# Optimization experiments

Hardware: AMD Instinct MI355X
Metric: run time of the kernel (lower is better)

Reference implementation:

```python
import jax, jax.numpy as jnp
import numpy as np

MARGIN = 0.5

def _pairwise_dist(x):
    # Euclidean cdist with grad-safe sqrt (diagonal is exactly zero).
    sq = jnp.sum(x * x, axis=1)
    d2 = sq[:, None] + sq[None, :] - 2.0 * (x @ x.T)
    d2 = jnp.maximum(d2, 0.0)
    safe = jnp.where(d2 > 0.0, d2, 1.0)
    return jnp.where(d2 > 0.0, jnp.sqrt(safe), 0.0)

def setup_inputs() -> dict:
    key = jax.random.key(0)
    k1, k2 = jax.random.split(key)
    embeddings = jax.random.normal(k1, (8192, 128), dtype=jnp.float32)
    labels = jax.random.randint(k2, (8192,), 0, 256, dtype=jnp.int64)
    return {"embeddings": embeddings, "labels": labels}

def reference(embeddings, labels):
    B = embeddings.shape[0]
    dist = _pairwise_dist(embeddings)                      # [B, B]
    same = labels[:, None] == labels[None, :]              # [B, B]
    eye = jnp.eye(B, dtype=bool)
    pos_mask = same & ~eye
    neg_mask = ~same
    neg_inf = jnp.float32(-jnp.inf)
    pos_inf = jnp.float32(jnp.inf)
    hardest_pos = jnp.max(jnp.where(pos_mask, dist, neg_inf), axis=1)  # [B]
    hardest_neg = jnp.min(jnp.where(neg_mask, dist, pos_inf), axis=1)  # [B]
    valid = jnp.any(pos_mask, axis=1) & jnp.any(neg_mask, axis=1)      # [B]
    per_anchor = jnp.maximum(hardest_pos - hardest_neg + MARGIN, 0.0)
    per_anchor = jnp.where(valid, per_anchor, 0.0)
    num = jnp.sum(valid.astype(jnp.float32))
    return jnp.sum(per_anchor) / jnp.maximum(num, 1.0)
```

## Files before the change

kernel.cpp:

```cpp
#include <hip/hip_runtime.h>
#include <hip/hip_bf16.h>
#include <stdint.h>


typedef __bf16 bf16x8 __attribute__((ext_vector_type(8)));
typedef float f32x4 __attribute__((ext_vector_type(4)));

constexpr int NB = 8192;
constexpr int ND = 128;
constexpr int BM = 256;
constexpr int BN = 64;
constexpr int SPLIT = 16;
constexpr int JRANGE = NB / SPLIT;
constexpr int NT = JRANGE / BN;

constexpr size_t OFF_XB  = 0;
constexpr size_t OFF_SQ  = (size_t)NB * ND * 2;
constexpr size_t OFF_LAB = OFF_SQ + (size_t)NB * 4;
constexpr size_t OFF_HP  = OFF_LAB + (size_t)NB * 4;
constexpr size_t OFF_HN  = OFF_HP + (size_t)SPLIT * NB * 4;
constexpr size_t OFF_ACC = OFF_HN + (size_t)SPLIT * NB * 4;

__device__ __forceinline__ unsigned short f2bf(float f) {
  union { float f; uint32_t u; } c; c.f = f;
  uint32_t u = c.u;
  u += 0x7fffu + ((u >> 16) & 1u);
  return (unsigned short)(u >> 16);
}

__global__ __launch_bounds__(256) void prep_kernel(
    const float* __restrict__ x, const int* __restrict__ labels,
    unsigned short* __restrict__ xb, float* __restrict__ sq,
    int* __restrict__ lab) {
  const int row = blockIdx.x * 4 + (threadIdx.x >> 6);
  const int lane = threadIdx.x & 63;
  const float2 v = *reinterpret_cast<const float2*>(x + (size_t)row * ND + lane * 2);
  ushort2 o;
  o.x = f2bf(v.x);
  o.y = f2bf(v.y);
  *reinterpret_cast<ushort2*>(xb + (size_t)row * ND + lane * 2) = o;
  float s = v.x * v.x + v.y * v.y;
#pragma unroll
  for (int m = 1; m < 64; m <<= 1) s += __shfl_xor(s, m);
  if (lane == 0) {
    sq[row] = s;
    lab[row] = labels[row];
  }
}

__global__ __launch_bounds__(256) void hard_kernel(
    const unsigned short* __restrict__ xb, const float* __restrict__ sq,
    const int* __restrict__ lab, float* __restrict__ hp_out,
    float* __restrict__ hn_out) {
  __shared__ __align__(16) char smem[2][BN * ND * 2];
  const int tid = threadIdx.x;
  const int lane = tid & 63;
  const int w = tid >> 6;
  const int rowbase = blockIdx.x * BM;
  const int jbase0 = blockIdx.y * JRANGE;

  const int c16 = lane & 15;
  const int g4 = lane >> 4;

  bf16x8 afrag[4][4];
#pragma unroll
  for (int rt = 0; rt < 4; ++rt) {
    const unsigned short* ap =
        xb + ((size_t)(rowbase + w * 64 + rt * 16 + c16)) * ND + g4 * 8;
#pragma unroll
    for (int kk = 0; kk < 4; ++kk)
      afrag[rt][kk] = *reinterpret_cast<const bf16x8*>(ap + kk * 32);
  }
  int labr[4][4];
#pragma unroll
  for (int rt = 0; rt < 4; ++rt)
#pragma unroll
    for (int r = 0; r < 4; ++r)
      labr[rt][r] = lab[rowbase + w * 64 + rt * 16 + g4 * 4 + r];

  float hp2[4][4], hn2[4][4];
#pragma unroll
  for (int rt = 0; rt < 4; ++rt)
#pragma unroll
    for (int r = 0; r < 4; ++r) {
      hp2[rt][r] = -__builtin_inff();
      hn2[rt][r] = __builtin_inff();
    }

  auto stage = [&](int buf, int tile) {
    const char* gbase = reinterpret_cast<const char*>(xb) +
                        ((size_t)(jbase0 + tile * BN)) * (ND * 2);
#pragma unroll
    for (int rnd = 0; rnd < 4; ++rnd) {
      const int L = rnd * 4096 + tid * 16;
      const int slot = (L >> 4) & 15;
      const int col = L >> 8;
      const int src = (L & ~0xF0) | ((slot ^ (col & 15)) << 4);
      __builtin_amdgcn_global_load_lds(
          (const __attribute__((address_space(1))) unsigned int*)(gbase + src),
          (__attribute__((address_space(3))) unsigned int*)(&smem[buf][L]),
          16, 0, 0);
    }
  };

  stage(0, 0);
  __syncthreads();

  for (int t = 0; t < NT; ++t) {
    if (t + 1 < NT) stage((t + 1) & 1, t + 1);
    const char* sb = smem[t & 1];
    const int jtile = jbase0 + t * BN;
#pragma unroll
    for (int jj = 0; jj < 4; ++jj) {
      const int jcol = jtile + jj * 16 + c16;
      const float sqc = sq[jcol];
      const int labc = lab[jcol];
      const int colL = jj * 16 + c16;

      bf16x8 bfrag[4];
#pragma unroll
      for (int kk = 0; kk < 4; ++kk) {
        const int kbyte = kk * 64 + g4 * 16;
        const int a = colL * 256 + (kbyte ^ (c16 << 4));
        bfrag[kk] = *reinterpret_cast<const bf16x8*>(sb + a);
      }

      f32x4 acc[4];
#pragma unroll
      for (int rt = 0; rt < 4; ++rt) acc[rt] = (f32x4){0.f, 0.f, 0.f, 0.f};
#pragma unroll
      for (int kk = 0; kk < 4; ++kk)
#pragma unroll
        for (int rt = 0; rt < 4; ++rt)
          acc[rt] = __builtin_amdgcn_mfma_f32_16x16x32_bf16(
              afrag[rt][kk], bfrag[kk], acc[rt], 0, 0, 0);

#pragma unroll
      for (int rt = 0; rt < 4; ++rt)
#pragma unroll
        for (int r = 0; r < 4; ++r) {
          const float tv = fmaf(-2.f, acc[rt][r], sqc);
          const bool same = (labc == labr[rt][r]);
          hp2[rt][r] = fmaxf(hp2[rt][r], same ? tv : -__builtin_inff());
          hn2[rt][r] = fminf(hn2[rt][r], same ? __builtin_inff() : tv);
        }
    }
    __syncthreads();
  }

#pragma unroll
  for (int rt = 0; rt < 4; ++rt)
#pragma unroll
    for (int r = 0; r < 4; ++r) {
      float p = hp2[rt][r], n = hn2[rt][r];
#pragma unroll
      for (int m = 1; m <= 8; m <<= 1) {
        p = fmaxf(p, __shfl_xor(p, m));
        n = fminf(n, __shfl_xor(n, m));
      }
      if (c16 == 0) {
        const int rg = rowbase + w * 64 + rt * 16 + g4 * 4 + r;
        hp_out[(size_t)blockIdx.y * NB + rg] = p;
        hn_out[(size_t)blockIdx.y * NB + rg] = n;
      }
    }
}

__global__ __launch_bounds__(256) void reduce_kernel(
    const float* __restrict__ hp, const float* __restrict__ hn,
    const float* __restrict__ sq, float* __restrict__ accum) {
  const int a = blockIdx.x * 256 + threadIdx.x;
  float p = -__builtin_inff(), n = __builtin_inff();
#pragma unroll
  for (int s = 0; s < SPLIT; ++s) {
    p = fmaxf(p, hp[(size_t)s * NB + a]);
    n = fminf(n, hn[(size_t)s * NB + a]);
  }
  const float sqa = sq[a];
  const float d2p = fmaxf(sqa + p, 0.f);
  const float d2n = fmaxf(sqa + n, 0.f);
  const bool valid = (d2p > 1.0f) && (n < 1e37f);
  float loss = valid ? fmaxf(sqrtf(d2p) - sqrtf(d2n) + 0.5f, 0.f) : 0.f;
  float cnt = valid ? 1.f : 0.f;
#pragma unroll
  for (int m = 1; m < 64; m <<= 1) {
    loss += __shfl_xor(loss, m);
    cnt += __shfl_xor(cnt, m);
  }
  __shared__ float ls[4], cs[4];
  const int w = threadIdx.x >> 6, lane = threadIdx.x & 63;
  if (lane == 0) { ls[w] = loss; cs[w] = cnt; }
  __syncthreads();
  if (threadIdx.x == 0) {
    atomicAdd(&accum[0], ls[0] + ls[1] + ls[2] + ls[3]);
    atomicAdd(&accum[1], cs[0] + cs[1] + cs[2] + cs[3]);
  }
}

__global__ void finalize_kernel(const float* __restrict__ accum,
                                float* __restrict__ out) {
  out[0] = accum[0] / fmaxf(accum[1], 1.f);
}

extern "C" void kernel_launch(void* const* d_in, const int* in_sizes, int n_in,
                              void* d_out, int out_size, void* d_ws,
                              size_t ws_size, hipStream_t stream) {
  const float* x = (const float*)d_in[0];
  const int* labels = (const int*)d_in[1];
  char* ws = (char*)d_ws;
  unsigned short* xb = (unsigned short*)(ws + OFF_XB);
  float* sq = (float*)(ws + OFF_SQ);
  int* lab = (int*)(ws + OFF_LAB);
  float* hp = (float*)(ws + OFF_HP);
  float* hn = (float*)(ws + OFF_HN);
  float* acc = (float*)(ws + OFF_ACC);

  hipMemsetAsync(acc, 0, 2 * sizeof(float), stream);
  prep_kernel<<<NB / 4, 256, 0, stream>>>(x, labels, xb, sq, lab);
  hard_kernel<<<dim3(NB / BM, SPLIT), 256, 0, stream>>>(xb, sq, lab, hp, hn);
  reduce_kernel<<<NB / 256, 256, 0, stream>>>(hp, hn, sq, acc);
  finalize_kernel<<<1, 1, 0, stream>>>(acc, (float*)d_out);
}
```

Measured before the change: 93.97 us.

## Fold memset and finalize into kernels, cache column metadata in LDS

The memset is removed by zeroing the accumulators inside prep_kernel. The finalize kernel is removed by having the last reduce block, found through an atomic counter, write the output. prep_kernel now uses float4 loads with 8 rows per block, and hard_kernel stages its column sq and label slices into shared memory and adds a launch_bounds occupancy hint. The aim is fewer launches and fewer scattered global loads in the inner loop, at the cost of some extra LDS and the register pressure the occupancy hint imposes.

```diff
diff --git a/kernel.cpp b/kernel.cpp
--- a/kernel.cpp
+++ b/kernel.cpp
@@ -31,28 +31,34 @@
 __global__ __launch_bounds__(256) void prep_kernel(
     const float* __restrict__ x, const int* __restrict__ labels,
     unsigned short* __restrict__ xb, float* __restrict__ sq,
-    int* __restrict__ lab) {
-  const int row = blockIdx.x * 4 + (threadIdx.x >> 6);
-  const int lane = threadIdx.x & 63;
-  const float2 v = *reinterpret_cast<const float2*>(x + (size_t)row * ND + lane * 2);
-  ushort2 o;
-  o.x = f2bf(v.x);
-  o.y = f2bf(v.y);
-  *reinterpret_cast<ushort2*>(xb + (size_t)row * ND + lane * 2) = o;
-  float s = v.x * v.x + v.y * v.y;
-#pragma unroll
-  for (int m = 1; m < 64; m <<= 1) s += __shfl_xor(s, m);
-  if (lane == 0) {
+    int* __restrict__ lab, float* __restrict__ acc, int* __restrict__ cnt) {
+  if (blockIdx.x == 0 && threadIdx.x == 0) {
+    acc[0] = 0.f;
+    acc[1] = 0.f;
+    *cnt = 0;
+  }
+  const int row = blockIdx.x * 8 + (threadIdx.x >> 5);
+  const int sub = threadIdx.x & 31;
+  const float4 v = *reinterpret_cast<const float4*>(x + (size_t)row * ND + sub * 4);
+  ushort4 o;
+  o.x = f2bf(v.x); o.y = f2bf(v.y); o.z = f2bf(v.z); o.w = f2bf(v.w);
+  *reinterpret_cast<ushort4*>(xb + (size_t)row * ND + sub * 4) = o;
+  float s = v.x * v.x + v.y * v.y + v.z * v.z + v.w * v.w;
+#pragma unroll
+  for (int m = 1; m < 32; m <<= 1) s += __shfl_xor(s, m);
+  if (sub == 0) {
     sq[row] = s;
     lab[row] = labels[row];
   }
 }
 
-__global__ __launch_bounds__(256) void hard_kernel(
+__global__ __launch_bounds__(256, 2) void hard_kernel(
     const unsigned short* __restrict__ xb, const float* __restrict__ sq,
     const int* __restrict__ lab, float* __restrict__ hp_out,
     float* __restrict__ hn_out) {
   __shared__ __align__(16) char smem[2][BN * ND * 2];
+  __shared__ float sql[JRANGE];
+  __shared__ int labl[JRANGE];
   const int tid = threadIdx.x;
   const int lane = tid & 63;
   const int w = tid >> 6;
@@ -61,31 +67,6 @@
 
   const int c16 = lane & 15;
   const int g4 = lane >> 4;
-
-  bf16x8 afrag[4][4];
-#pragma unroll
-  for (int rt = 0; rt < 4; ++rt) {
-    const unsigned short* ap =
-        xb + ((size_t)(rowbase + w * 64 + rt * 16 + c16)) * ND + g4 * 8;
-#pragma unroll
-    for (int kk = 0; kk < 4; ++kk)
-      afrag[rt][kk] = *reinterpret_cast<const bf16x8*>(ap + kk * 32);
-  }
-  int labr[4][4];
-#pragma unroll
-  for (int rt = 0; rt < 4; ++rt)
-#pragma unroll
-    for (int r = 0; r < 4; ++r)
-      labr[rt][r] = lab[rowbase + w * 64 + rt * 16 + g4 * 4 + r];
-
-  float hp2[4][4], hn2[4][4];
-#pragma unroll
-  for (int rt = 0; rt < 4; ++rt)
-#pragma unroll
-    for (int r = 0; r < 4; ++r) {
-      hp2[rt][r] = -__builtin_inff();
-      hn2[rt][r] = __builtin_inff();
-    }
 
   auto stage = [&](int buf, int tile) {
     const char* gbase = reinterpret_cast<const char*>(xb) +
@@ -104,17 +85,49 @@
   };
 
   stage(0, 0);
+  {
+    const int i2 = tid * 2;
+    *reinterpret_cast<float2*>(&sql[i2]) =
+        *reinterpret_cast<const float2*>(&sq[jbase0 + i2]);
+    *reinterpret_cast<int2*>(&labl[i2]) =
+        *reinterpret_cast<const int2*>(&lab[jbase0 + i2]);
+  }
+
+  bf16x8 afrag[4][4];
+#pragma unroll
+  for (int rt = 0; rt < 4; ++rt) {
+    const unsigned short* ap =
+        xb + ((size_t)(rowbase + w * 64 + rt * 16 + c16)) * ND + g4 * 8;
+#pragma unroll
+    for (int kk = 0; kk < 4; ++kk)
+      afrag[rt][kk] = *reinterpret_cast<const bf16x8*>(ap + kk * 32);
+  }
+  int labr[4][4];
+#pragma unroll
+  for (int rt = 0; rt < 4; ++rt)
+#pragma unroll
+    for (int r = 0; r < 4; ++r)
+      labr[rt][r] = lab[rowbase + w * 64 + rt * 16 + g4 * 4 + r];
+
+  float hp2[4][4], hn2[4][4];
+#pragma unroll
+  for (int rt = 0; rt < 4; ++rt)
+#pragma unroll
+    for (int r = 0; r < 4; ++r) {
+      hp2[rt][r] = -__builtin_inff();
+      hn2[rt][r] = __builtin_inff();
+    }
+
   __syncthreads();
 
   for (int t = 0; t < NT; ++t) {
     if (t + 1 < NT) stage((t + 1) & 1, t + 1);
     const char* sb = smem[t & 1];
-    const int jtile = jbase0 + t * BN;
 #pragma unroll
     for (int jj = 0; jj < 4; ++jj) {
-      const int jcol = jtile + jj * 16 + c16;
-      const float sqc = sq[jcol];
-      const int labc = lab[jcol];
+      const int jidx = t * BN + jj * 16 + c16;
+      const float sqc = sql[jidx];
+      const int labc = labl[jidx];
       const int colL = jj * 16 + c16;
 
       bf16x8 bfrag[4];
@@ -168,7 +181,8 @@
 
 __global__ __launch_bounds__(256) void reduce_kernel(
     const float* __restrict__ hp, const float* __restrict__ hn,
-    const float* __restrict__ sq, float* __restrict__ accum) {
+    const float* __restrict__ sq, float* __restrict__ acc,
+    int* __restrict__ cnt_done, float* __restrict__ out) {
   const int a = blockIdx.x * 256 + threadIdx.x;
   float p = -__builtin_inff(), n = __builtin_inff();
 #pragma unroll
@@ -181,25 +195,27 @@
   const float d2n = fmaxf(sqa + n, 0.f);
   const bool valid = (d2p > 1.0f) && (n < 1e37f);
   float loss = valid ? fmaxf(sqrtf(d2p) - sqrtf(d2n) + 0.5f, 0.f) : 0.f;
-  float cnt = valid ? 1.f : 0.f;
+  float c = valid ? 1.f : 0.f;
 #pragma unroll
   for (int m = 1; m < 64; m <<= 1) {
     loss += __shfl_xor(loss, m);
-    cnt += __shfl_xor(cnt, m);
+    c += __shfl_xor(c, m);
   }
   __shared__ float ls[4], cs[4];
   const int w = threadIdx.x >> 6, lane = threadIdx.x & 63;
-  if (lane == 0) { ls[w] = loss; cs[w] = cnt; }
+  if (lane == 0) { ls[w] = loss; cs[w] = c; }
   __syncthreads();
   if (threadIdx.x == 0) {
-    atomicAdd(&accum[0], ls[0] + ls[1] + ls[2] + ls[3]);
-    atomicAdd(&accum[1], cs[0] + cs[1] + cs[2] + cs[3]);
-  }
-}
-
-__global__ void finalize_kernel(const float* __restrict__ accum,
-                                float* __restrict__ out) {
-  out[0] = accum[0] / fmaxf(accum[1], 1.f);
+    atomicAdd(&acc[0], ls[0] + ls[1] + ls[2] + ls[3]);
+    atomicAdd(&acc[1], cs[0] + cs[1] + cs[2] + cs[3]);
+    __threadfence();
+    const int old = atomicAdd(cnt_done, 1);
+    if (old == (NB / 256) - 1) {
+      const float l = atomicAdd(&acc[0], 0.0f);
+      const float nvalid = atomicAdd(&acc[1], 0.0f);
+      out[0] = l / fmaxf(nvalid, 1.f);
+    }
+  }
 }
 
 extern "C" void kernel_launch(void* const* d_in, const int* in_sizes, int n_in,
@@ -214,10 +230,10 @@
   float* hp = (float*)(ws + OFF_HP);
   float* hn = (float*)(ws + OFF_HN);
   float* acc = (float*)(ws + OFF_ACC);
-
-  hipMemsetAsync(acc, 0, 2 * sizeof(float), stream);
-  prep_kernel<<<NB / 4, 256, 0, stream>>>(x, labels, xb, sq, lab);
+  int* cnt = (int*)(ws + OFF_ACC + 8);
+
+  prep_kernel<<<NB / 8, 256, 0, stream>>>(x, labels, xb, sq, lab, acc, cnt);
   hard_kernel<<<dim3(NB / BM, SPLIT), 256, 0, stream>>>(xb, sq, lab, hp, hn);
-  reduce_kernel<<<NB / 256, 256, 0, stream>>>(hp, hn, sq, acc);
-  finalize_kernel<<<1, 1, 0, stream>>>(acc, (float*)d_out);
-}
+  reduce_kernel<<<NB / 256, 256, 0, stream>>>(hp, hn, sq, acc, cnt,
+                                              (float*)d_out);
+}
```

After: 89.65 us. -4.6%, faster.
